# Optimization experiments

Measured on AMD Instinct MI355X. Metric: run time of the kernel, lower is better.

The kernel has to match this reference:

```python
import jax, jax.numpy as jnp
import numpy as np

B, FEAT, H, V = 512, 2048, 512, 100
STEPS = 200  # TEXT_MAX_LEN - 1
SOS = 0      # char2idx['<SOS>']


def setup_inputs() -> dict:
    key = jax.random.key(0)
    ks = jax.random.split(key, 8)
    s = 0.02  # small init keeps tanh/sigmoid in a sane range over 200 steps
    return {
        "feat": jax.random.normal(ks[0], (B, FEAT), jnp.float32),
        "w_hp": jax.random.normal(ks[1], (FEAT, H), jnp.float32) * s,
        "b_hp": jnp.zeros((H,), jnp.float32),
        "embed": jax.random.normal(ks[2], (V, H), jnp.float32) * s,
        "w_ih": jax.random.normal(ks[3], (3 * H, H), jnp.float32) * s,
        "w_hh": jax.random.normal(ks[4], (3 * H, H), jnp.float32) * s,
        "b_ih": jnp.zeros((3 * H,), jnp.float32),
        "b_hh": jnp.zeros((3 * H,), jnp.float32),
        "w_proj": jax.random.normal(ks[5], (H, V), jnp.float32) * s,
        "b_proj": jnp.zeros((V,), jnp.float32),
    }


def _gru_cell(x, h, w_ih, w_hh, b_ih, b_hh):
    # PyTorch GRU cell: gates ordered (reset, update, new)
    gi = x @ w_ih.T + b_ih            # [B, 3H]
    gh = h @ w_hh.T + b_hh            # [B, 3H]
    i_r, i_z, i_n = jnp.split(gi, 3, axis=-1)
    h_r, h_z, h_n = jnp.split(gh, 3, axis=-1)
    r = jax.nn.sigmoid(i_r + h_r)
    z = jax.nn.sigmoid(i_z + h_z)
    n = jnp.tanh(i_n + r * h_n)
    return (1.0 - z) * n + z * h      # new hidden = output


def reference(feat, w_hp, b_hp, embed, w_ih, w_hh, b_ih, b_hh, w_proj, b_proj):
    # hidden init = hidden_proj(resnet pooled feature)  -> [B, H]
    h0 = feat @ w_hp + b_hp
    # first input = embedding of <SOS>, broadcast over batch
    x0 = jnp.broadcast_to(embed[SOS], (feat.shape[0], embed.shape[1]))

    def step(carry, _):
        h, x = carry
        h_new = _gru_cell(x, h, w_ih, w_hh, b_ih, b_hh)
        # output feeds back as next step's input (out -> inp)
        return (h_new, h_new), h_new

    _, outs = jax.lax.scan(step, (h0, x0), None, length=STEPS)  # [T, B, H]
    res = jnp.transpose(outs, (1, 0, 2))                        # [B, T, H]
    logits = res @ w_proj + b_proj                              # [B, T, V]
    return jnp.transpose(logits, (0, 2, 1))                     # [B, V, T]
```

## Files before the change

### kernel.cpp

```cpp
#include <hip/hip_runtime.h>

#define Bsz  512
#define FEAT 2048
#define Hd   512
#define Vd   100
#define Td   200
#define Gd   2048

typedef __bf16 bf16;
typedef __bf16 bf16x8 __attribute__((ext_vector_type(8)));
typedef float  f32x4  __attribute__((ext_vector_type(4)));

__device__ bf16  g_hbuf[Td + 1][Bsz][Hd];
__device__ bf16  g_hping[2][Bsz][Hd];
__device__ bf16  g_wt0[Gd][Hd];
__device__ bf16  g_wt1[Gd][Hd];
__device__ float g_bias0[Gd];
__device__ float g_bias1[Gd];
__device__ bf16  g_featbf[Bsz][FEAT];
__device__ bf16  g_whpt[Hd][FEAT];
__device__ bf16  g_wprojt[112][Hd];
__device__ float g_gi0[3 * Hd];
__device__ unsigned g_flags[8][32];
__device__ unsigned g_bar[8][32];
__device__ unsigned g_xcd[256];

template <int OFF>
__device__ __forceinline__ bf16x8 ld_b16x8_cohere(const void* p) {
  bf16x8 r;
  asm volatile("global_load_dwordx4 %0, %1, off offset:%2 sc0 sc1"
               : "=&v"(r) : "v"(p), "i"(OFF) : "memory");
  return r;
}
template <int OFF>
__device__ __forceinline__ bf16x8 ld_b16x8_l2(const void* p) {
  bf16x8 r;
  asm volatile("global_load_dwordx4 %0, %1, off offset:%2 sc1"
               : "=&v"(r) : "v"(p), "i"(OFF) : "memory");
  return r;
}
template <int OFF>
__device__ __forceinline__ void st_u16_cohere(void* p, unsigned short v) {
  asm volatile("global_store_short %0, %1, off offset:%2 sc0 sc1"
               :: "v"(p), "v"(v), "i"(OFF) : "memory");
}
__device__ __forceinline__ void st_u32_cohere(void* p, unsigned v) {
  asm volatile("global_store_dword %0, %1, off sc0 sc1" :: "v"(p), "v"(v) : "memory");
}
__device__ __forceinline__ unsigned ld_u32_cohere(const void* p) {
  unsigned r;
  asm volatile("global_load_dword %0, %1, off sc0 sc1\n\ts_waitcnt vmcnt(0)"
               : "=&v"(r) : "v"(p) : "memory");
  return r;
}
__device__ __forceinline__ unsigned atomic_rd(unsigned* p) {
  unsigned r;
  asm volatile("global_atomic_add %0, %1, %2, off sc0\n\ts_waitcnt vmcnt(0)"
               : "=&v"(r) : "v"(p), "v"(0u) : "memory");
  return r;
}
__device__ __forceinline__ void atomic_inc(unsigned* p) {
  asm volatile("global_atomic_add %0, %1, off" :: "v"(p), "v"(1u) : "memory");
}
__device__ __forceinline__ void wait_vm0() { asm volatile("s_waitcnt vmcnt(0)" ::: "memory"); }
__device__ __forceinline__ void wait_vm8() { asm volatile("s_waitcnt vmcnt(8)" ::: "memory"); }

#define LDA16(arr, base) do {                                                   \
  arr[0]  = ld_b16x8_cohere<0>(base);   arr[1]  = ld_b16x8_cohere<64>(base);    \
  arr[2]  = ld_b16x8_cohere<128>(base); arr[3]  = ld_b16x8_cohere<192>(base);   \
  arr[4]  = ld_b16x8_cohere<256>(base); arr[5]  = ld_b16x8_cohere<320>(base);   \
  arr[6]  = ld_b16x8_cohere<384>(base); arr[7]  = ld_b16x8_cohere<448>(base);   \
  arr[8]  = ld_b16x8_cohere<512>(base); arr[9]  = ld_b16x8_cohere<576>(base);   \
  arr[10] = ld_b16x8_cohere<640>(base); arr[11] = ld_b16x8_cohere<704>(base);   \
  arr[12] = ld_b16x8_cohere<768>(base); arr[13] = ld_b16x8_cohere<832>(base);   \
  arr[14] = ld_b16x8_cohere<896>(base); arr[15] = ld_b16x8_cohere<960>(base);   \
} while (0)

#define LDA16_L2(arr, base) do {                                                \
  arr[0]  = ld_b16x8_l2<0>(base);   arr[1]  = ld_b16x8_l2<64>(base);            \
  arr[2]  = ld_b16x8_l2<128>(base); arr[3]  = ld_b16x8_l2<192>(base);           \
  arr[4]  = ld_b16x8_l2<256>(base); arr[5]  = ld_b16x8_l2<320>(base);           \
  arr[6]  = ld_b16x8_l2<384>(base); arr[7]  = ld_b16x8_l2<448>(base);           \
  arr[8]  = ld_b16x8_l2<512>(base); arr[9]  = ld_b16x8_l2<576>(base);           \
  arr[10] = ld_b16x8_l2<640>(base); arr[11] = ld_b16x8_l2<704>(base);           \
  arr[12] = ld_b16x8_l2<768>(base); arr[13] = ld_b16x8_l2<832>(base);           \
  arr[14] = ld_b16x8_l2<896>(base); arr[15] = ld_b16x8_l2<960>(base);           \
} while (0)

__device__ __forceinline__ float sigmoidf_(float x) {
  x = fminf(fmaxf(x, -30.f), 30.f);
  return 1.f / (1.f + __expf(-x));
}
__device__ __forceinline__ float tanhf_(float x) {
  x = fminf(fmaxf(x, -15.f), 15.f);
  float e = __expf(2.f * x);
  return (e - 1.f) / (e + 1.f);
}

__device__ __forceinline__ void group_barrier(int rg, int cg, unsigned phase) {
  wait_vm0();
  __syncthreads();
  if (threadIdx.x == 0) st_u32_cohere(&g_flags[rg][cg], phase);
  if (threadIdx.x < 64) {
    const unsigned* fp = &g_flags[rg][threadIdx.x & 31];
    while (ld_u32_cohere(fp) < phase) __builtin_amdgcn_s_sleep(1);
  }
  __syncthreads();
}


__global__ void k_conv_feat(const float* feat) {
  int i = blockIdx.x * 256 + threadIdx.x;
  if (i < Bsz * FEAT) ((bf16*)g_featbf)[i] = (bf16)feat[i];
  if (blockIdx.x == 0) {
    ((unsigned*)g_flags)[threadIdx.x] = 0u;
    ((unsigned*)g_bar)[threadIdx.x] = 0u;
    g_xcd[threadIdx.x] = 0xffffffffu;
  }
}

__global__ void k_gi0(const float* embed, const float* w_ih, const float* b_ih) {
  int j = blockIdx.x;
  const float* wr = w_ih + (size_t)j * Hd;
  float s = 0.f;
  for (int k = threadIdx.x; k < Hd; k += 64) s += embed[k] * wr[k];
#pragma unroll
  for (int off = 32; off > 0; off >>= 1) s += __shfl_down(s, off);
  if (threadIdx.x == 0) g_gi0[j] = s + b_ih[j];
}

__global__ void k_build_wt1(const float* w_ih, const float* w_hh,
                            const float* b_ih, const float* b_hh) {
  int c = blockIdx.x;
  int j = (c >> 6) * 16 + (c & 15);
  int f = (c >> 4) & 3;
  const float* s1 = nullptr; const float* s2 = nullptr; float bias;
  if (f == 0)      { s1 = w_ih + (size_t)j * Hd;            s2 = w_hh + (size_t)j * Hd;            bias = b_ih[j] + b_hh[j]; }
  else if (f == 1) { s1 = w_ih + (size_t)(Hd + j) * Hd;     s2 = w_hh + (size_t)(Hd + j) * Hd;     bias = b_ih[Hd + j] + b_hh[Hd + j]; }
  else if (f == 2) { s1 = w_ih + (size_t)(2 * Hd + j) * Hd;                                        bias = b_ih[2 * Hd + j]; }
  else             { s1 = w_hh + (size_t)(2 * Hd + j) * Hd;                                        bias = b_hh[2 * Hd + j]; }
  for (int k = threadIdx.x; k < Hd; k += 256) {
    float v = s1[k] + (s2 ? s2[k] : 0.f);
    g_wt1[c][k] = (bf16)v;
  }
  if (threadIdx.x == 0) g_bias1[c] = bias;
}

__global__ void k_build_wt0(const float* w_hh, const float* b_hh) {
  int c = blockIdx.x;
  int j = (c >> 6) * 16 + (c & 15);
  int f = (c >> 4) & 3;
  const float* s1 = nullptr; float bias;
  if (f == 0)      { s1 = w_hh + (size_t)j * Hd;            bias = g_gi0[j] + b_hh[j]; }
  else if (f == 1) { s1 = w_hh + (size_t)(Hd + j) * Hd;     bias = g_gi0[Hd + j] + b_hh[Hd + j]; }
  else if (f == 2) {                                        bias = g_gi0[2 * Hd + j]; }
  else             { s1 = w_hh + (size_t)(2 * Hd + j) * Hd; bias = b_hh[2 * Hd + j]; }
  for (int k = threadIdx.x; k < Hd; k += 256)
    g_wt0[c][k] = (bf16)(s1 ? s1[k] : 0.f);
  if (threadIdx.x == 0) g_bias0[c] = bias;
}

__global__ void k_build_whpt(const float* w_hp) {
  int n = blockIdx.x;
  for (int k = threadIdx.x; k < FEAT; k += 256)
    g_whpt[n][k] = (bf16)w_hp[(size_t)k * Hd + n];
}

__global__ void k_build_wprojt(const float* w_proj) {
  int v = blockIdx.x;
  for (int k = threadIdx.x; k < Hd; k += 256)
    g_wprojt[v][k] = (bf16)(v < Vd ? w_proj[(size_t)k * Vd + v] : 0.f);
}

__global__ __launch_bounds__(256, 1) void k_gru_seq(const float* b_hp) {
  const int bid = blockIdx.x;
  const int rg = bid & 7;
  const int cg = bid >> 3;
  const int w = threadIdx.x >> 6, l = threadIdx.x & 63;
  const int m = l & 15;
  const int ksub = (l >> 4) * 8;
  const int colb = cg * 64;
  const int arow = rg * 64 + w * 16 + m;
  const int orow = rg * 64 + w * 16 + (l >> 4) * 4;
  const int hcol = cg * 16 + m;
  __shared__ int s_fast;

  bf16x8 Bw[64];
#pragma unroll
  for (int f = 0; f < 4; f++)
#pragma unroll
    for (int k0 = 0; k0 < 16; k0++)
      Bw[f * 16 + k0] = *(const bf16x8*)&g_wt1[colb + f * 16 + m][k0 * 32 + ksub];

  float b0v[4], b1v[4];
#pragma unroll
  for (int f = 0; f < 4; f++) {
    b0v[f] = g_bias0[colb + f * 16 + m];
    b1v[f] = g_bias1[colb + f * 16 + m];
  }

  unsigned xcc;
  asm volatile("s_getreg_b32 %0, hwreg(HW_REG_XCC_ID)" : "=s"(xcc));
  if (threadIdx.x == 0) st_u32_cohere(&g_xcd[bid], xcc);
  group_barrier(rg, cg, 1u);
  if (threadIdx.x < 64) {
    unsigned peer = ld_u32_cohere(&g_xcd[rg + 8 * (threadIdx.x & 31)]);
    unsigned long long bal = __ballot(peer == xcc);
    if (threadIdx.x == 0) s_fast = (bal == ~0ull) ? 1 : 0;
  }
  __syncthreads();
  const bool fast = (s_fast != 0);

  float hcarry[4];
  {
    f32x4 acc = {0.f, 0.f, 0.f, 0.f};
#pragma unroll 4
    for (int k0 = 0; k0 < FEAT; k0 += 32) {
      bf16x8 a = *(const bf16x8*)&g_featbf[arow][k0 + ksub];
      bf16x8 b = *(const bf16x8*)&g_whpt[hcol][k0 + ksub];
      acc = __builtin_amdgcn_mfma_f32_16x16x32_bf16(a, b, acc, 0, 0, 0);
    }
    float bhp = b_hp[hcol];
    bf16* ph = &g_hbuf[0][orow][hcol];
    bf16* pp = &g_hping[0][orow][hcol];
    unsigned short us[4];
#pragma unroll
    for (int i = 0; i < 4; i++) {
      bf16 hv = (bf16)(acc[i] + bhp);
      hcarry[i] = (float)hv;
      us[i] = __builtin_bit_cast(unsigned short, hv);
    }
    if (fast) {
#pragma unroll
      for (int i = 0; i < 4; i++) {
        pp[i * Hd] = __builtin_bit_cast(bf16, us[i]);
        ph[i * Hd] = __builtin_bit_cast(bf16, us[i]);
      }
    } else {
      char* pc = (char*)ph;
      st_u16_cohere<0>(pc, us[0]);    st_u16_cohere<1024>(pc, us[1]);
      st_u16_cohere<2048>(pc, us[2]); st_u16_cohere<3072>(pc, us[3]);
    }
  }

  if (fast) {
    unsigned* cnt = &g_bar[rg][0];
    wait_vm0();
    __syncthreads();
    if (threadIdx.x == 0) {
      atomic_inc(cnt);
      while (atomic_rd(cnt) < 32u) __builtin_amdgcn_s_sleep(1);
    }
    __syncthreads();

    for (int t = 0; t < Td; t++) {
      bf16x8 a[16];
      const char* Ap = (const char*)&g_hping[t & 1][arow][ksub];
      LDA16_L2(a, Ap);

      f32x4 acc[4], acc2[4];
#pragma unroll
      for (int f = 0; f < 4; f++) {
        float bv = (t == 0) ? b0v[f] : b1v[f];
        acc[f]  = (f32x4){bv, bv, bv, bv};
        acc2[f] = (f32x4){0.f, 0.f, 0.f, 0.f};
      }
      wait_vm8(); __builtin_amdgcn_sched_barrier(0);
      if (t == 0) {
#pragma unroll
        for (int k0 = 0; k0 < 8; k0++)
#pragma unroll
          for (int f = 0; f < 4; f++) {
            bf16x8 b = *(const bf16x8*)&g_wt0[colb + f * 16 + m][k0 * 32 + ksub];
            acc[f] = __builtin_amdgcn_mfma_f32_16x16x32_bf16(a[k0], b, acc[f], 0, 0, 0);
          }
        wait_vm0(); __builtin_amdgcn_sched_barrier(0);
#pragma unroll
        for (int k0 = 8; k0 < 16; k0++)
#pragma unroll
          for (int f = 0; f < 4; f++) {
            bf16x8 b = *(const bf16x8*)&g_wt0[colb + f * 16 + m][k0 * 32 + ksub];
            acc2[f] = __builtin_amdgcn_mfma_f32_16x16x32_bf16(a[k0], b, acc2[f], 0, 0, 0);
          }
      } else {
#pragma unroll
        for (int k0 = 0; k0 < 8; k0++)
#pragma unroll
          for (int f = 0; f < 4; f++)
            acc[f] = __builtin_amdgcn_mfma_f32_16x16x32_bf16(a[k0], Bw[f * 16 + k0], acc[f], 0, 0, 0);
        wait_vm0(); __builtin_amdgcn_sched_barrier(0);
#pragma unroll
        for (int k0 = 8; k0 < 16; k0++)
#pragma unroll
          for (int f = 0; f < 4; f++)
            acc2[f] = __builtin_amdgcn_mfma_f32_16x16x32_bf16(a[k0], Bw[f * 16 + k0], acc2[f], 0, 0, 0);
      }

      bf16 hv4[4];
      bf16* pp = &g_hping[(t + 1) & 1][orow][hcol];
#pragma unroll
      for (int i = 0; i < 4; i++) {
        float r = sigmoidf_(acc[0][i] + acc2[0][i]);
        float z = sigmoidf_(acc[1][i] + acc2[1][i]);
        float n = tanhf_((acc[2][i] + acc2[2][i]) + r * (acc[3][i] + acc2[3][i]));
        float hn = (1.f - z) * n + z * hcarry[i];
        bf16 hv = (bf16)hn;
        hcarry[i] = (float)hv;
        hv4[i] = hv;
        pp[i * Hd] = hv;
      }
      wait_vm0();

      bf16* ph = &g_hbuf[t + 1][orow][hcol];
#pragma unroll
      for (int i = 0; i < 4; i++) ph[i * Hd] = hv4[i];

      if (t < Td - 1) {
        __syncthreads();
        if (threadIdx.x == 0) {
          atomic_inc(cnt);
          unsigned tgt = 32u * (unsigned)(t + 2);
          while (atomic_rd(cnt) < tgt) __builtin_amdgcn_s_sleep(1);
        }
        __syncthreads();
      }
    }
  } else {
    group_barrier(rg, cg, 2u);
    for (int t = 0; t < Td; t++) {
      bf16x8 a[16];
      const char* Ap = (const char*)&g_hbuf[t][arow][ksub];
      LDA16(a, Ap);

      f32x4 acc[4];
#pragma unroll
      for (int f = 0; f < 4; f++) {
        float bv = (t == 0) ? b0v[f] : b1v[f];
        acc[f] = (f32x4){bv, bv, bv, bv};
      }
      if (t == 0) {
        wait_vm0(); __builtin_amdgcn_sched_barrier(0);
#pragma unroll
        for (int k0 = 0; k0 < 16; k0++)
#pragma unroll
          for (int f = 0; f < 4; f++) {
            bf16x8 b = *(const bf16x8*)&g_wt0[colb + f * 16 + m][k0 * 32 + ksub];
            acc[f] = __builtin_amdgcn_mfma_f32_16x16x32_bf16(a[k0], b, acc[f], 0, 0, 0);
          }
      } else {
        wait_vm8(); __builtin_amdgcn_sched_barrier(0);
#pragma unroll
        for (int k0 = 0; k0 < 8; k0++)
#pragma unroll
          for (int f = 0; f < 4; f++)
            acc[f] = __builtin_amdgcn_mfma_f32_16x16x32_bf16(a[k0], Bw[f * 16 + k0], acc[f], 0, 0, 0);
        wait_vm0(); __builtin_amdgcn_sched_barrier(0);
#pragma unroll
        for (int k0 = 8; k0 < 16; k0++)
#pragma unroll
          for (int f = 0; f < 4; f++)
            acc[f] = __builtin_amdgcn_mfma_f32_16x16x32_bf16(a[k0], Bw[f * 16 + k0], acc[f], 0, 0, 0);
      }

      char* pb = (char*)&g_hbuf[t + 1][orow][hcol];
      unsigned short us[4];
#pragma unroll
      for (int i = 0; i < 4; i++) {
        float r = sigmoidf_(acc[0][i]);
        float z = sigmoidf_(acc[1][i]);
        float n = tanhf_(acc[2][i] + r * acc[3][i]);
        float hn = (1.f - z) * n + z * hcarry[i];
        bf16 hv = (bf16)hn;
        hcarry[i] = (float)hv;
        us[i] = __builtin_bit_cast(unsigned short, hv);
      }
      st_u16_cohere<0>(pb, us[0]);    st_u16_cohere<1024>(pb, us[1]);
      st_u16_cohere<2048>(pb, us[2]); st_u16_cohere<3072>(pb, us[3]);

      if (t < Td - 1) group_barrier(rg, cg, (unsigned)(t + 3));
    }
  }
  wait_vm0();
}

__global__ __launch_bounds__(256) void k_proj(const float* b_proj, float* out) {
  int b = blockIdx.x;
  int w = threadIdx.x >> 6, l = threadIdx.x & 63;
  int tt = blockIdx.y * 4 + w;
  if (tt > 12) return;
  int m = l & 15, ksub = (l >> 4) * 8;
  int tcol = tt * 16 + m;
  int trow = (tcol < Td ? tcol : Td - 1) + 1;

  f32x4 acc[7];
#pragma unroll
  for (int f = 0; f < 7; f++)
#pragma unroll
    for (int i = 0; i < 4; i++) {
      int v = f * 16 + (l >> 4) * 4 + i;
      acc[f][i] = (v < Vd) ? b_proj[v] : 0.f;
    }

  bf16x8 bb[16];
  const bf16* Bp = &g_hbuf[trow][b][ksub];
#pragma unroll
  for (int k0 = 0; k0 < 16; k0++) bb[k0] = *(const bf16x8*)(Bp + k0 * 32);

#pragma unroll
  for (int k0 = 0; k0 < 16; k0++)
#pragma unroll
    for (int f = 0; f < 7; f++) {
      bf16x8 afrag = *(const bf16x8*)&g_wprojt[f * 16 + m][k0 * 32 + ksub];
      acc[f] = __builtin_amdgcn_mfma_f32_16x16x32_bf16(afrag, bb[k0], acc[f], 0, 0, 0);
    }

  if (tcol < Td) {
#pragma unroll
    for (int f = 0; f < 7; f++)
#pragma unroll
      for (int i = 0; i < 4; i++) {
        int v = f * 16 + (l >> 4) * 4 + i;
        if (v < Vd) out[((size_t)b * Vd + v) * Td + tcol] = acc[f][i];
      }
  }
}

extern "C" void kernel_launch(void* const* d_in, const int* in_sizes, int n_in,
                              void* d_out, int out_size, void* d_ws, size_t ws_size,
                              hipStream_t stream) {
  const float* feat   = (const float*)d_in[0];
  const float* w_hp   = (const float*)d_in[1];
  const float* b_hp   = (const float*)d_in[2];
  const float* embed  = (const float*)d_in[3];
  const float* w_ih   = (const float*)d_in[4];
  const float* w_hh   = (const float*)d_in[5];
  const float* b_ih   = (const float*)d_in[6];
  const float* b_hh   = (const float*)d_in[7];
  const float* w_proj = (const float*)d_in[8];
  const float* b_proj = (const float*)d_in[9];
  float* out = (float*)d_out;

  hipLaunchKernelGGL(k_conv_feat, dim3((Bsz * FEAT) / 256), dim3(256), 0, stream, feat);
  hipLaunchKernelGGL(k_gi0, dim3(3 * Hd), dim3(64), 0, stream, embed, w_ih, b_ih);
  hipLaunchKernelGGL(k_build_wt1, dim3(Gd), dim3(256), 0, stream, w_ih, w_hh, b_ih, b_hh);
  hipLaunchKernelGGL(k_build_wt0, dim3(Gd), dim3(256), 0, stream, w_hh, b_hh);
  hipLaunchKernelGGL(k_build_whpt, dim3(Hd), dim3(256), 0, stream, w_hp);
  hipLaunchKernelGGL(k_build_wprojt, dim3(112), dim3(256), 0, stream, w_proj);
  hipLaunchKernelGGL(k_gru_seq, dim3(256), dim3(256), 0, stream, b_hp);
  hipLaunchKernelGGL(k_proj, dim3(Bsz, 4), dim3(256), 0, stream, b_proj, out);
}
```

Baseline: 1.050 ms.

## Repartition GRU blocks into 32 row groups of 8 blocks for smaller barriers

Changes the block-to-tile mapping so each block owns 16 batch rows and 256 gate columns, with the four waves splitting columns. Row groups now span 8 blocks instead of 32, so the per-step group barrier waits on 8 arrivals, and the spin loop drops s_sleep in favour of busy-polling. The fast path also stops writing the initial hidden state into g_hbuf. This cuts barrier latency on the serial 200-step recurrence. In exchange each block reloads A rows differently per wave, busy-polling adds memory traffic, and the XCD-locality check has to find 8 co-located peers.

```diff
diff --git a/kernel.cpp b/kernel.cpp
--- a/kernel.cpp
+++ b/kernel.cpp
@@ -21,8 +21,8 @@
 __device__ bf16  g_whpt[Hd][FEAT];
 __device__ bf16  g_wprojt[112][Hd];
 __device__ float g_gi0[3 * Hd];
-__device__ unsigned g_flags[8][32];
-__device__ unsigned g_bar[8][32];
+__device__ unsigned g_flags[32][8];
+__device__ unsigned g_dbar[32][16];
 __device__ unsigned g_xcd[256];
 
 template <int OFF>
@@ -102,7 +102,7 @@
   __syncthreads();
   if (threadIdx.x == 0) st_u32_cohere(&g_flags[rg][cg], phase);
   if (threadIdx.x < 64) {
-    const unsigned* fp = &g_flags[rg][threadIdx.x & 31];
+    const unsigned* fp = &g_flags[rg][threadIdx.x & 7];
     while (ld_u32_cohere(fp) < phase) __builtin_amdgcn_s_sleep(1);
   }
   __syncthreads();
@@ -114,7 +114,8 @@
   if (i < Bsz * FEAT) ((bf16*)g_featbf)[i] = (bf16)feat[i];
   if (blockIdx.x == 0) {
     ((unsigned*)g_flags)[threadIdx.x] = 0u;
-    ((unsigned*)g_bar)[threadIdx.x] = 0u;
+    ((unsigned*)g_dbar)[threadIdx.x] = 0u;
+    ((unsigned*)g_dbar)[256 + threadIdx.x] = 0u;
     g_xcd[threadIdx.x] = 0xffffffffu;
   }
 }
@@ -174,15 +175,15 @@
 
 __global__ __launch_bounds__(256, 1) void k_gru_seq(const float* b_hp) {
   const int bid = blockIdx.x;
-  const int rg = bid & 7;
-  const int cg = bid >> 3;
+  const int rg = (bid & 7) * 4 + ((bid >> 3) & 3);
+  const int cg = bid >> 5;
   const int w = threadIdx.x >> 6, l = threadIdx.x & 63;
   const int m = l & 15;
   const int ksub = (l >> 4) * 8;
-  const int colb = cg * 64;
-  const int arow = rg * 64 + w * 16 + m;
-  const int orow = rg * 64 + w * 16 + (l >> 4) * 4;
-  const int hcol = cg * 16 + m;
+  const int colb = (cg * 4 + w) * 64;
+  const int arow = rg * 16 + m;
+  const int srow = rg * 16 + (l >> 4) * 4;
+  const int hcol = (cg * 4 + w) * 16 + m;
   __shared__ int s_fast;
 
   bf16x8 Bw[64];
@@ -204,9 +205,10 @@
   if (threadIdx.x == 0) st_u32_cohere(&g_xcd[bid], xcc);
   group_barrier(rg, cg, 1u);
   if (threadIdx.x < 64) {
-    unsigned peer = ld_u32_cohere(&g_xcd[rg + 8 * (threadIdx.x & 31)]);
+    int c = threadIdx.x & 7;
+    unsigned peer = ld_u32_cohere(&g_xcd[(rg >> 2) + ((rg & 3) << 3) + (c << 5)]);
     unsigned long long bal = __ballot(peer == xcc);
-    if (threadIdx.x == 0) s_fast = (bal == ~0ull) ? 1 : 0;
+    if (threadIdx.x == 0) s_fast = ((bal & 0xffull) == 0xffull) ? 1 : 0;
   }
   __syncthreads();
   const bool fast = (s_fast != 0);
@@ -221,8 +223,6 @@
       acc = __builtin_amdgcn_mfma_f32_16x16x32_bf16(a, b, acc, 0, 0, 0);
     }
     float bhp = b_hp[hcol];
-    bf16* ph = &g_hbuf[0][orow][hcol];
-    bf16* pp = &g_hping[0][orow][hcol];
     unsigned short us[4];
 #pragma unroll
     for (int i = 0; i < 4; i++) {
@@ -231,25 +231,23 @@
       us[i] = __builtin_bit_cast(unsigned short, hv);
     }
     if (fast) {
-#pragma unroll
-      for (int i = 0; i < 4; i++) {
-        pp[i * Hd] = __builtin_bit_cast(bf16, us[i]);
-        ph[i * Hd] = __builtin_bit_cast(bf16, us[i]);
-      }
+      bf16* pp = &g_hping[0][srow][hcol];
+#pragma unroll
+      for (int i = 0; i < 4; i++) pp[i * Hd] = __builtin_bit_cast(bf16, us[i]);
     } else {
-      char* pc = (char*)ph;
+      char* pc = (char*)&g_hbuf[0][srow][hcol];
       st_u16_cohere<0>(pc, us[0]);    st_u16_cohere<1024>(pc, us[1]);
       st_u16_cohere<2048>(pc, us[2]); st_u16_cohere<3072>(pc, us[3]);
     }
   }
 
   if (fast) {
-    unsigned* cnt = &g_bar[rg][0];
+    unsigned* cnt = &g_dbar[rg][0];
     wait_vm0();
     __syncthreads();
     if (threadIdx.x == 0) {
       atomic_inc(cnt);
-      while (atomic_rd(cnt) < 32u) __builtin_amdgcn_s_sleep(1);
+      while (atomic_rd(cnt) < 8u) { }
     }
     __syncthreads();
 
@@ -297,7 +295,7 @@
       }
 
       bf16 hv4[4];
-      bf16* pp = &g_hping[(t + 1) & 1][orow][hcol];
+      bf16* pp = &g_hping[(t + 1) & 1][srow][hcol];
 #pragma unroll
       for (int i = 0; i < 4; i++) {
         float r = sigmoidf_(acc[0][i] + acc2[0][i]);
@@ -311,7 +309,7 @@
       }
       wait_vm0();
 
-      bf16* ph = &g_hbuf[t + 1][orow][hcol];
+      bf16* ph = &g_hbuf[t + 1][srow][hcol];
 #pragma unroll
       for (int i = 0; i < 4; i++) ph[i * Hd] = hv4[i];
 
@@ -319,8 +317,8 @@
         __syncthreads();
         if (threadIdx.x == 0) {
           atomic_inc(cnt);
-          unsigned tgt = 32u * (unsigned)(t + 2);
-          while (atomic_rd(cnt) < tgt) __builtin_amdgcn_s_sleep(1);
+          unsigned tgt = 8u * (unsigned)(t + 2);
+          while (atomic_rd(cnt) < tgt) { }
         }
         __syncthreads();
       }
@@ -362,7 +360,7 @@
             acc[f] = __builtin_amdgcn_mfma_f32_16x16x32_bf16(a[k0], Bw[f * 16 + k0], acc[f], 0, 0, 0);
       }
 
-      char* pb = (char*)&g_hbuf[t + 1][orow][hcol];
+      char* pb = (char*)&g_hbuf[t + 1][srow][hcol];
       unsigned short us[4];
 #pragma unroll
       for (int i = 0; i < 4; i++) {
```

Measured after the change: 954.4 us. 1.1x faster.
